# Kernel tuning notes

Measured on AMD Instinct MI355X. Metric: run time of the kernel, lower is better.

The kernel has to match this reference:

```python
import jax, jax.numpy as jnp
import numpy as np

SCALE = 0.08838834764831845  # 1/sqrt(head_dim=128)


def setup_inputs() -> dict:
    key = jax.random.key(0)
    k0, k1, k2 = jax.random.split(key, 3)
    T, H, HKV, D = 8192, 16, 4, 128        # total_tokens, heads, kv heads, head_dim
    NB, BS = 64, 256                        # num_blocks, block_size (NB*BS == T)
    B, BPS = 4, 8                           # batch, blocks per sequence (seq_len = BPS*BS = 2048)
    return {
        "q": jax.random.normal(k0, (T, H, D), jnp.float32),
        "k": jax.random.normal(k1, (T, HKV, D), jnp.float32),
        "v": jax.random.normal(k2, (T, HKV, D), jnp.float32),
        "k_cache": jnp.zeros((NB, BS, HKV, D), jnp.float32),
        "v_cache": jnp.zeros((NB, BS, HKV, D), jnp.float32),
        "slot_mapping": jnp.arange(T, dtype=jnp.int32),
        "block_tables": jnp.arange(B * BPS, dtype=jnp.int32).reshape(B, BPS),
    }


def reference(q, k, v, k_cache, v_cache, slot_mapping, block_tables):
    T, H, D = q.shape
    HKV = k.shape[1]
    NB, BS = k_cache.shape[0], k_cache.shape[1]
    num_slots = NB * BS

    # --- paged KV-cache store (store_kv_cache_kernel): slot -1 means skip ---
    idx = jnp.where(slot_mapping >= 0, slot_mapping, num_slots)  # out-of-range -> dropped
    kc = k_cache.reshape(num_slots, HKV, D).at[idx].set(k, mode="drop")
    vc = v_cache.reshape(num_slots, HKV, D).at[idx].set(v, mode="drop")

    # --- prefill with block tables: read K/V back through the paged cache ---
    B, BPS = block_tables.shape
    S = BPS * BS  # per-sequence length (equal-length ragged batch)
    k_seq = kc.reshape(NB, BS, HKV, D)[block_tables].reshape(B, S, HKV, D)
    v_seq = vc.reshape(NB, BS, HKV, D)[block_tables].reshape(B, S, HKV, D)

    qb = q.reshape(B, S, H, D)
    G = H // HKV  # GQA group size
    kx = jnp.repeat(k_seq, G, axis=2)  # [B,S,H,D]
    vx = jnp.repeat(v_seq, G, axis=2)

    scores = jnp.einsum("bqhd,bkhd->bhqk", qb, kx) * SCALE
    causal = jnp.tril(jnp.ones((S, S), dtype=bool))
    scores = jnp.where(causal, scores, jnp.finfo(scores.dtype).min)
    p = jax.nn.softmax(scores, axis=-1)
    o = jnp.einsum("bhqk,bkhd->bqhd", p, vx)
    return o.reshape(T, H, D)
```

## Files before the change

### kernel.cpp

```cpp
#include <hip/hip_runtime.h>
#include <hip/hip_bf16.h>

typedef unsigned short u16;
typedef unsigned int u32;
typedef __attribute__((ext_vector_type(8))) short bf16x8;
typedef __attribute__((ext_vector_type(4))) float f32x4;

constexpr int T = 8192, H = 16, HKV = 4, D = 128, NB = 64, BS = 256, B = 4, BPS = 8;
constexpr int S = 2048, G = 4;
constexpr float CEXP = 0.08838834764831845f * 1.4426950408889634f;

constexpr int BQ = 128;
constexpr int BK = 32;
constexpr int PPAD = 36;
constexpr int TOK = 32;
constexpr int QF = 128;
constexpr int QROW = 132;

__device__ __forceinline__ float e2(float x) { return __builtin_amdgcn_exp2f(x); }

__device__ __forceinline__ u32 pk_bf16(float a, float b) {
  __hip_bfloat162 h = __float22bfloat162_rn(float2{a, b});
  u32 r; __builtin_memcpy(&r, &h, 4); return r;
}

__device__ __forceinline__ void dma16(const u16* g, u16* l) {
  __builtin_amdgcn_global_load_lds(
      (const __attribute__((address_space(1))) void*)g,
      (__attribute__((address_space(3))) void*)l, 16, 0, 0);
}

__global__ __launch_bounds__(256) void store_kv(
    const float* __restrict__ k, const float* __restrict__ v,
    u16* __restrict__ kcb, u16* __restrict__ vcb, const int* __restrict__ slot) {
  __shared__ int ls[TOK];
  __shared__ int fastflag;
  __shared__ u16 ldv[TOK * QROW];
  int tid = threadIdx.x;
  int t0 = blockIdx.x * TOK;
  int base = blockIdx.y * QF;
  if (tid < TOK) ls[tid] = slot[t0 + tid];
  if (tid == 0) fastflag = 1;
  __syncthreads();
  int s0 = ls[0];
  if (tid < TOK) {
    bool ok = (ls[tid] == s0 + tid);
    if (tid == 0) ok = ok && (s0 >= 0) && ((s0 & 31) == 0) && (s0 + TOK <= NB * BS);
    if (!ok) fastflag = 0;
  }
#pragma unroll
  for (int i = 0; i < 4; ++i) {
    int f = tid + i * 256;
    int t = f >> 5, c4 = f & 31;
    int st = ls[t];
    float4 k4 = *(const float4*)(k + (size_t)(t0 + t) * (HKV * D) + base + c4 * 4);
    float4 v4 = *(const float4*)(v + (size_t)(t0 + t) * (HKV * D) + base + c4 * 4);
    if (st >= 0 && st < NB * BS) {
      uint2 kb = {pk_bf16(k4.x, k4.y), pk_bf16(k4.z, k4.w)};
      *(uint2*)(kcb + (size_t)st * (HKV * D) + base + c4 * 4) = kb;
    }
    u32* ld = (u32*)&ldv[t * QROW + c4 * 4];
    ld[0] = pk_bf16(v4.x, v4.y);
    ld[1] = pk_bf16(v4.z, v4.w);
  }
  __syncthreads();
  if (fastflag) {
    int blk = s0 >> 8, pos0 = s0 & 255;
#pragma unroll
    for (int i = 0; i < 2; ++i) {
      int f = tid + i * 256;
      int row = f >> 2, c8 = f & 3;
      union { uint4 q; u16 s[8]; } o;
#pragma unroll
      for (int j = 0; j < 8; ++j) o.s[j] = ldv[(c8 * 8 + j) * QROW + row];
      *(uint4*)(vcb + ((size_t)blk * (HKV * D) + base + row) * BS + pos0 + c8 * 8) = o.q;
    }
  } else {
#pragma unroll
    for (int i = 0; i < 16; ++i) {
      int f = tid + i * 256;
      int t = f >> 7, row = f & 127;
      int st = ls[t];
      if (st >= 0 && st < NB * BS)
        vcb[((size_t)(st >> 8) * (HKV * D) + base + row) * BS + (st & 255)] =
            ldv[t * QROW + row];
    }
  }
}

__global__ __launch_bounds__(256, 2) void attn(
    const float* __restrict__ q, const u16* __restrict__ kcb,
    const u16* __restrict__ vcb, const int* __restrict__ bt,
    float* __restrict__ out) {
  __shared__ u16 Kl[2][32 * 128];
  __shared__ u16 Vl[2][128 * 32];
  __shared__ u16 lp[4][2][16 * PPAD];

  int tid = threadIdx.x;
  int lane = tid & 63;
  int w = __builtin_amdgcn_readfirstlane(tid >> 6);
  int col = lane & 15, quad = lane >> 4;

  int i = (int)blockIdx.x;
  int xcd = i & 7;
  int r_ = i >> 3;
  int j = r_ >> 3;
  int inner = r_ & 7;
  int p = (xcd << 1) | (inner >> 2);
  int b = p >> 2, hkv = p & 3;
  int h = hkv * G + (inner & 3);

  const int* btrow = bt + b * BPS;
  int bt0 = __builtin_amdgcn_readfirstlane(btrow[0]);
  int bt1 = __builtin_amdgcn_readfirstlane(btrow[1]);
  int bt2 = __builtin_amdgcn_readfirstlane(btrow[2]);
  int bt3 = __builtin_amdgcn_readfirstlane(btrow[3]);
  int bt4 = __builtin_amdgcn_readfirstlane(btrow[4]);
  int bt5 = __builtin_amdgcn_readfirstlane(btrow[5]);
  int bt6 = __builtin_amdgcn_readfirstlane(btrow[6]);
  int bt7 = __builtin_amdgcn_readfirstlane(btrow[7]);
  auto selblk = [&](int jj) -> int {
    int s01 = (jj & 1) ? bt1 : bt0, s23 = (jj & 1) ? bt3 : bt2;
    int s45 = (jj & 1) ? bt5 : bt4, s67 = (jj & 1) ? bt7 : bt6;
    int s03 = (jj & 2) ? s23 : s01, s47 = (jj & 2) ? s67 : s45;
    return (jj & 4) ? s47 : s03;
  };

  u32 kOff[2], vOff[2], dmaDst[2];
#pragma unroll
  for (int ii = 0; ii < 2; ++ii) {
    int rK = (w * 2 + ii) * 4 + (lane >> 4), cK = lane & 15;
    kOff[ii] = (u32)(rK * (HKV * D) + ((cK ^ (rK & 7)) * 8));
    int rV = (w * 2 + ii) * 16 + (lane >> 2), cV = lane & 3;
    vOff[ii] = (u32)(rV * BS + ((cV ^ ((rV >> 2) & 3)) * 8));
    dmaDst[ii] = (u32)((w * 2 + ii) * 512);
  }

  auto phase = [&](int qt) {
    int qbase = qt * BQ;

    bf16x8 qf[2][4];
#pragma unroll
    for (int mt = 0; mt < 2; ++mt) {
      int qrow = qbase + w * 32 + mt * 16 + col;
      const float* qp = q + ((size_t)(b * S + qrow) * H + h) * D;
#pragma unroll
      for (int kc = 0; kc < 4; ++kc) {
        float4 a0 = *(const float4*)(qp + kc * 32 + quad * 8);
        float4 a1 = *(const float4*)(qp + kc * 32 + quad * 8 + 4);
        union { bf16x8 v; u32 s[4]; } u;
        u.s[0] = pk_bf16(a0.x, a0.y); u.s[1] = pk_bf16(a0.z, a0.w);
        u.s[2] = pk_bf16(a1.x, a1.y); u.s[3] = pk_bf16(a1.z, a1.w);
        qf[mt][kc] = u.v;
      }
    }

    f32x4 oacc[2][8];
#pragma unroll
    for (int mt = 0; mt < 2; ++mt)
#pragma unroll
      for (int dt = 0; dt < 8; ++dt) oacc[mt][dt] = (f32x4){0.f, 0.f, 0.f, 0.f};
    float lsum[2][4] = {{0.f, 0.f, 0.f, 0.f}, {0.f, 0.f, 0.f, 0.f}};

    int q_hi = qbase + w * 32 + 31;
    int kend = qbase + BQ;

    const u16* kb = kcb + ((size_t)(bt0 * BS) * HKV + hkv) * D;
    const u16* vb = vcb + ((size_t)bt0 * HKV + hkv) * (size_t)(D * BS);

    asm volatile("s_waitcnt vmcnt(0)" ::: "memory");
    __builtin_amdgcn_sched_barrier(0);
    __builtin_amdgcn_s_barrier();
    __builtin_amdgcn_sched_barrier(0);
    dma16(kb + kOff[0], &Kl[0][dmaDst[0]]);
    dma16(kb + kOff[1], &Kl[0][dmaDst[1]]);
    dma16(vb + vOff[0], &Vl[0][dmaDst[0]]);
    dma16(vb + vOff[1], &Vl[0][dmaDst[1]]);

    int buf = 0;
    for (int kt = 0; kt < kend; kt += BK) {
      asm volatile("s_waitcnt vmcnt(0)" ::: "memory");
      __builtin_amdgcn_sched_barrier(0);
      __builtin_amdgcn_s_barrier();
      __builtin_amdgcn_sched_barrier(0);

      {
        int ktn = kt + BK;
        if (ktn < kend) {
          if ((ktn & 255) == 0) {
            int blkN = selblk(ktn >> 8);
            kb = kcb + ((size_t)(blkN * BS) * HKV + hkv) * D;
            vb = vcb + ((size_t)blkN * HKV + hkv) * (size_t)(D * BS);
          } else {
            kb += BK * HKV * D;
            vb += BK;
          }
        }
        dma16(kb + kOff[0], &Kl[buf ^ 1][dmaDst[0]]);
        dma16(kb + kOff[1], &Kl[buf ^ 1][dmaDst[1]]);
        dma16(vb + vOff[0], &Vl[buf ^ 1][dmaDst[0]]);
        dma16(vb + vOff[1], &Vl[buf ^ 1][dmaDst[1]]);
      }

      bool act = (kt <= q_hi);
      if (act) {
        f32x4 sf[2][2];
        __builtin_amdgcn_s_setprio(1);
#pragma unroll
        for (int n = 0; n < 2; ++n) {
          sf[0][n] = (f32x4){0.f, 0.f, 0.f, 0.f};
          sf[1][n] = (f32x4){0.f, 0.f, 0.f, 0.f};
          int krow = n * 16 + col;
#pragma unroll
          for (int kc = 0; kc < 4; ++kc) {
            bf16x8 kf = *(const bf16x8*)&Kl[buf][krow * 128 + (((kc * 4 + quad) ^ (col & 7)) * 8)];
            sf[0][n] = __builtin_amdgcn_mfma_f32_16x16x32_bf16(qf[0][kc], kf, sf[0][n], 0, 0, 0);
            sf[1][n] = __builtin_amdgcn_mfma_f32_16x16x32_bf16(qf[1][kc], kf, sf[1][n], 0, 0, 0);
          }
        }
        __builtin_amdgcn_s_setprio(0);

#pragma unroll
        for (int mt = 0; mt < 2; ++mt) {
          int q_lo = qbase + w * 32 + mt * 16;
          bool nm = (kt + 31 > q_lo);
#pragma unroll
          for (int r = 0; r < 4; ++r) {
            float p0 = e2(sf[mt][0][r] * CEXP);
            float p1 = e2(sf[mt][1][r] * CEXP);
            if (nm) {
              int qg = q_lo + quad * 4 + r;
              if (kt + col > qg) p0 = 0.f;
              if (kt + 16 + col > qg) p1 = 0.f;
            }
            lsum[mt][r] += p0 + p1;
            u32 pb = pk_bf16(p0, p1);
            u16* dst = &lp[w][mt][(quad * 4 + r) * PPAD + col];
            dst[0] = (u16)(pb & 0xffffu);
            dst[16] = (u16)(pb >> 16);
          }
        }

        bf16x8 pf0 = *(const bf16x8*)&lp[w][0][col * PPAD + quad * 8];
        bf16x8 pf1 = *(const bf16x8*)&lp[w][1][col * PPAD + quad * 8];
        __builtin_amdgcn_s_setprio(1);
#pragma unroll
        for (int dt = 0; dt < 8; ++dt) {
          bf16x8 vf = *(const bf16x8*)&Vl[buf][(dt * 16 + col) * 32 + ((quad ^ ((col >> 2) & 3)) * 8)];
          oacc[0][dt] = __builtin_amdgcn_mfma_f32_16x16x32_bf16(pf0, vf, oacc[0][dt], 0, 0, 0);
          oacc[1][dt] = __builtin_amdgcn_mfma_f32_16x16x32_bf16(pf1, vf, oacc[1][dt], 0, 0, 0);
        }
        __builtin_amdgcn_s_setprio(0);
      }
      buf ^= 1;
    }

#pragma unroll
    for (int mt = 0; mt < 2; ++mt)
#pragma unroll
      for (int r = 0; r < 4; ++r) {
        float l = lsum[mt][r];
        l += __shfl_xor(l, 1); l += __shfl_xor(l, 2);
        l += __shfl_xor(l, 4); l += __shfl_xor(l, 8);
        float inv = 1.f / l;
        int qg = qbase + w * 32 + mt * 16 + quad * 4 + r;
        size_t ob = ((size_t)(b * S + qg) * H + h) * D;
#pragma unroll
        for (int dt = 0; dt < 8; ++dt)
          out[ob + dt * 16 + col] = oacc[mt][dt][r] * inv;
      }
  };

  phase(15 - j);
  phase(j);

  asm volatile("s_waitcnt vmcnt(0)" ::: "memory");
}

extern "C" void kernel_launch(void* const* d_in, const int* in_sizes, int n_in,
                              void* d_out, int out_size, void* d_ws, size_t ws_size,
                              hipStream_t stream) {
  const float* q = (const float*)d_in[0];
  const float* k = (const float*)d_in[1];
  const float* v = (const float*)d_in[2];
  const int* slot = (const int*)d_in[5];
  const int* bt = (const int*)d_in[6];
  float* out = (float*)d_out;

  size_t need = (size_t)T * HKV * D * sizeof(u16);
  u16* kcb; u16* vcb;
  if (ws_size >= 2 * need) {
    kcb = (u16*)d_ws;
    vcb = (u16*)d_ws + (need / sizeof(u16));
  } else {
    kcb = (u16*)d_in[3];
    vcb = (u16*)d_in[4];
  }

  dim3 sgrid(T / TOK, 4);
  store_kv<<<sgrid, 256, 0, stream>>>(k, v, kcb, vcb, slot);
  attn<<<dim3((S / (2 * BQ)) * H * B), 256, 0, stream>>>(q, kcb, vcb, bt, out);
}
```

Measured before the change: 270.6 us.

## Compute S transposed and reshuffle P in registers via permlane swaps

Swaps the MFMA operands for the QK^T product so scores come out transposed, putting each query row on a lane's column. The P fragment for the PV MFMA is then built in registers with v_permlane32_swap and ds_swizzle instead of being written to and read back from a per-wave LDS staging buffer. This removes the LDS round trip and its 16-bit scattered stores, and simplifies the row-sum reduction. In exchange it adds cross-lane permute instructions and selects, and the masking logic and final normalization shuffles change.

```diff
diff --git a/kernel.cpp b/kernel.cpp
--- a/kernel.cpp
+++ b/kernel.cpp
@@ -12,7 +12,6 @@
 
 constexpr int BQ = 128;
 constexpr int BK = 32;
-constexpr int PPAD = 36;
 constexpr int TOK = 32;
 constexpr int QF = 128;
 constexpr int QROW = 132;
@@ -22,6 +21,10 @@
 __device__ __forceinline__ u32 pk_bf16(float a, float b) {
   __hip_bfloat162 h = __float22bfloat162_rn(float2{a, b});
   u32 r; __builtin_memcpy(&r, &h, 4); return r;
+}
+
+__device__ __forceinline__ void pl32(u32& x, u32& y) {
+  asm("v_permlane32_swap_b32 %0, %1" : "+v"(x), "+v"(y));
 }
 
 __device__ __forceinline__ void dma16(const u16* g, u16* l) {
@@ -94,12 +97,12 @@
     float* __restrict__ out) {
   __shared__ u16 Kl[2][32 * 128];
   __shared__ u16 Vl[2][128 * 32];
-  __shared__ u16 lp[4][2][16 * PPAD];
 
   int tid = threadIdx.x;
   int lane = tid & 63;
   int w = __builtin_amdgcn_readfirstlane(tid >> 6);
   int col = lane & 15, quad = lane >> 4;
+  bool qodd = (quad & 1);
 
   int i = (int)blockIdx.x;
   int xcd = i & 7;
@@ -160,7 +163,7 @@
     for (int mt = 0; mt < 2; ++mt)
 #pragma unroll
       for (int dt = 0; dt < 8; ++dt) oacc[mt][dt] = (f32x4){0.f, 0.f, 0.f, 0.f};
-    float lsum[2][4] = {{0.f, 0.f, 0.f, 0.f}, {0.f, 0.f, 0.f, 0.f}};
+    float lsum[2] = {0.f, 0.f};
 
     int q_hi = qbase + w * 32 + 31;
     int kend = qbase + BQ;
@@ -214,41 +217,54 @@
 #pragma unroll
           for (int kc = 0; kc < 4; ++kc) {
             bf16x8 kf = *(const bf16x8*)&Kl[buf][krow * 128 + (((kc * 4 + quad) ^ (col & 7)) * 8)];
-            sf[0][n] = __builtin_amdgcn_mfma_f32_16x16x32_bf16(qf[0][kc], kf, sf[0][n], 0, 0, 0);
-            sf[1][n] = __builtin_amdgcn_mfma_f32_16x16x32_bf16(qf[1][kc], kf, sf[1][n], 0, 0, 0);
+            sf[0][n] = __builtin_amdgcn_mfma_f32_16x16x32_bf16(kf, qf[0][kc], sf[0][n], 0, 0, 0);
+            sf[1][n] = __builtin_amdgcn_mfma_f32_16x16x32_bf16(kf, qf[1][kc], sf[1][n], 0, 0, 0);
           }
         }
         __builtin_amdgcn_s_setprio(0);
 
+        bf16x8 pf[2];
 #pragma unroll
         for (int mt = 0; mt < 2; ++mt) {
           int q_lo = qbase + w * 32 + mt * 16;
+          int qg = q_lo + col;
           bool nm = (kt + 31 > q_lo);
-#pragma unroll
-          for (int r = 0; r < 4; ++r) {
-            float p0 = e2(sf[mt][0][r] * CEXP);
-            float p1 = e2(sf[mt][1][r] * CEXP);
-            if (nm) {
-              int qg = q_lo + quad * 4 + r;
-              if (kt + col > qg) p0 = 0.f;
-              if (kt + 16 + col > qg) p1 = 0.f;
+          float pv[2][4];
+#pragma unroll
+          for (int n = 0; n < 2; ++n)
+#pragma unroll
+            for (int r = 0; r < 4; ++r) {
+              float pp = e2(sf[mt][n][r] * CEXP);
+              if (nm && (kt + n * 16 + quad * 4 + r > qg)) pp = 0.f;
+              pv[n][r] = pp;
             }
-            lsum[mt][r] += p0 + p1;
-            u32 pb = pk_bf16(p0, p1);
-            u16* dst = &lp[w][mt][(quad * 4 + r) * PPAD + col];
-            dst[0] = (u16)(pb & 0xffffu);
-            dst[16] = (u16)(pb >> 16);
-          }
+          lsum[mt] += ((pv[0][0] + pv[0][1]) + (pv[0][2] + pv[0][3])) +
+                      ((pv[1][0] + pv[1][1]) + (pv[1][2] + pv[1][3]));
+          u32 w0 = pk_bf16(pv[0][0], pv[0][1]);
+          u32 w1 = pk_bf16(pv[0][2], pv[0][3]);
+          u32 w2 = pk_bf16(pv[1][0], pv[1][1]);
+          u32 w3 = pk_bf16(pv[1][2], pv[1][3]);
+          u32 a0 = w0, a1 = w2, b0 = w1, b1 = w3;
+          pl32(a0, a1);
+          pl32(b0, b1);
+          u32 sx = qodd ? a0 : a1;
+          u32 sy = qodd ? b0 : b1;
+          u32 rx = __builtin_amdgcn_ds_swizzle(sx, 0x401F);
+          u32 ry = __builtin_amdgcn_ds_swizzle(sy, 0x401F);
+          union { bf16x8 v; u32 s[4]; } pfu;
+          pfu.s[0] = qodd ? rx : a0;
+          pfu.s[1] = qodd ? ry : b0;
+          pfu.s[2] = qodd ? a1 : rx;
+          pfu.s[3] = qodd ? b1 : ry;
+          pf[mt] = pfu.v;
         }
 
-        bf16x8 pf0 = *(const bf16x8*)&lp[w][0][col * PPAD + quad * 8];
-        bf16x8 pf1 = *(const bf16x8*)&lp[w][1][col * PPAD + quad * 8];
         __builtin_amdgcn_s_setprio(1);
 #pragma unroll
         for (int dt = 0; dt < 8; ++dt) {
           bf16x8 vf = *(const bf16x8*)&Vl[buf][(dt * 16 + col) * 32 + ((quad ^ ((col >> 2) & 3)) * 8)];
-          oacc[0][dt] = __builtin_amdgcn_mfma_f32_16x16x32_bf16(pf0, vf, oacc[0][dt], 0, 0, 0);
-          oacc[1][dt] = __builtin_amdgcn_mfma_f32_16x16x32_bf16(pf1, vf, oacc[1][dt], 0, 0, 0);
+          oacc[0][dt] = __builtin_amdgcn_mfma_f32_16x16x32_bf16(pf[0], vf, oacc[0][dt], 0, 0, 0);
+          oacc[1][dt] = __builtin_amdgcn_mfma_f32_16x16x32_bf16(pf[1], vf, oacc[1][dt], 0, 0, 0);
         }
         __builtin_amdgcn_s_setprio(0);
       }
@@ -256,19 +272,22 @@
     }
 
 #pragma unroll
-    for (int mt = 0; mt < 2; ++mt)
+    for (int mt = 0; mt < 2; ++mt) {
+      float l = lsum[mt];
+      l += __shfl_xor(l, 16);
+      l += __shfl_xor(l, 32);
+      float inv = 1.f / l;
 #pragma unroll
       for (int r = 0; r < 4; ++r) {
-        float l = lsum[mt][r];
-        l += __shfl_xor(l, 1); l += __shfl_xor(l, 2);
-        l += __shfl_xor(l, 4); l += __shfl_xor(l, 8);
-        float inv = 1.f / l;
+        float invr = __shfl(inv, quad * 4 + r);
         int qg = qbase + w * 32 + mt * 16 + quad * 4 + r;
         size_t ob = ((size_t)(b * S + qg) * H + h) * D;
 #pragma unroll
         for (int dt = 0; dt < 8; ++dt)
-          out[ob + dt * 16 + col] = oacc[mt][dt][r] * inv;
+          out[ob + dt * 16 + col] = oacc[mt][dt][r] * invr;
       }
+      lsum[mt] = 0.f;
+    }
   };
 
   phase(15 - j);
```

Measured after the change: 268.7 us. Within noise of the previous version (-0.7%).
